# Performance work log

Measured on AMD Instinct MI355X. Metric: run time of the kernel, lower is better.

## Reference

```python
import jax, jax.numpy as jnp
import numpy as np

D_IN = 1024
D_OUT = 1024
SEQ = 4096


def setup_inputs() -> dict:
    key = jax.random.key(0)
    kx, kq, kk, kv = jax.random.split(key, 4)
    s = 1.0 / np.sqrt(D_IN)
    return {
        "x": jax.random.normal(kx, (SEQ, D_IN), dtype=jnp.float32),
        # torch Linear weights: shape [d_out, d_in], y = x @ W.T
        "Wq": jax.random.uniform(kq, (D_OUT, D_IN), jnp.float32, -s, s),
        "Wk": jax.random.uniform(kk, (D_OUT, D_IN), jnp.float32, -s, s),
        "Wv": jax.random.uniform(kv, (D_OUT, D_IN), jnp.float32, -s, s),
    }


def reference(x, Wq, Wk, Wv):
    # QKV projections (no bias)
    q = x @ Wq.T  # [N, d_out]
    k = x @ Wk.T
    v = x @ Wv.T
    scale = 1.0 / jnp.sqrt(jnp.asarray(k.shape[-1], x.dtype))
    att = jax.nn.softmax((q @ k.T) * scale, axis=-1)  # [N, N]
    return att @ v  # [N, d_out]
```

## Files before the change

### kernel.cpp

```cpp
#include <hip/hip_runtime.h>
#include <hip/hip_bf16.h>
#include <math.h>

typedef __attribute__((ext_vector_type(8))) short short8;
typedef __attribute__((ext_vector_type(4))) float floatx4;

static __device__ __forceinline__ unsigned short f2bf(float f) {
    union { float f; unsigned int u; } a; a.f = f;
    unsigned int u = a.u;
    return (unsigned short)((u + 0x7FFFu + ((u >> 16) & 1u)) >> 16);
}

static __device__ __forceinline__ void cvt8(const float* __restrict__ src,
                                            unsigned short* __restrict__ dst, int i) {
    float4 v0 = *(const float4*)(src + i);
    float4 v1 = *(const float4*)(src + i + 4);
    ushort4 o0, o1;
    o0.x = f2bf(v0.x); o0.y = f2bf(v0.y); o0.z = f2bf(v0.z); o0.w = f2bf(v0.w);
    o1.x = f2bf(v1.x); o1.y = f2bf(v1.y); o1.z = f2bf(v1.z); o1.w = f2bf(v1.w);
    *(ushort4*)(dst + i) = o0;
    *(ushort4*)(dst + i + 4) = o1;
}

__global__ __launch_bounds__(256)
void cvt_f32_bf16(const float* __restrict__ src, unsigned short* __restrict__ dst, int n) {
    int i = (blockIdx.x * 256 + threadIdx.x) * 8;
    if (i < n) cvt8(src, dst, i);
}

struct W3 { const float* s[3]; unsigned short* d[3]; };
__global__ __launch_bounds__(256)
void cvt_w3(W3 a, int n) {
    int i = (blockIdx.x * 256 + threadIdx.x) * 8;
    if (i < n) cvt8(a.s[blockIdx.z], a.d[blockIdx.z], i);
}

__global__ __launch_bounds__(256)
void zero_f32(float* __restrict__ p) { p[blockIdx.x * 256 + threadIdx.x] = 0.f; }

template<int BM, int BN, int TI, int TJ, int WCOLS>
__device__ __forceinline__ void gemm_core(const unsigned short* __restrict__ A,
                                          const unsigned short* __restrict__ B,
                                          int lda, int k_begin, int k_end,
                                          unsigned short* sA, unsigned short* sB,
                                          floatx4 (&acc)[TI][TJ],
                                          int bm, int bn)
{
    const int t    = threadIdx.x;
    const int wave = t >> 6;
    const int lane = t & 63;
    const int wm = (wave / WCOLS) * (TI * 16);
    const int wn = (wave % WCOLS) * (TJ * 16);

    const int srow   = t >> 3;
    const int schunk = t & 7;
    const int gchunk = schunk ^ (srow & 7);
    const int lm  = lane & 15;
    const int swz = lm & 7;

    for (int k0 = k_begin; k0 < k_end; k0 += 64) {
        __syncthreads();
        #pragma unroll
        for (int r = 0; r < BM / 32; r++) {
            const unsigned short* gA =
                A + (size_t)(bm + srow + r * 32) * lda + k0 + gchunk * 8;
            __builtin_amdgcn_global_load_lds(
                (const __attribute__((address_space(1))) void*)gA,
                (__attribute__((address_space(3))) void*)((char*)sA + wave * 1024 + r * 4096),
                16, 0, 0);
        }
        #pragma unroll
        for (int r = 0; r < BN / 32; r++) {
            const unsigned short* gB =
                B + (size_t)(bn + srow + r * 32) * lda + k0 + gchunk * 8;
            __builtin_amdgcn_global_load_lds(
                (const __attribute__((address_space(1))) void*)gB,
                (__attribute__((address_space(3))) void*)((char*)sB + wave * 1024 + r * 4096),
                16, 0, 0);
        }
        __syncthreads();

        #pragma unroll
        for (int kk = 0; kk < 64; kk += 32) {
            const int c  = (kk >> 3) + (lane >> 4);
            const int ce = ((c ^ swz) << 3);
            short8 a_frag[TI], b_frag[TJ];
            #pragma unroll
            for (int i = 0; i < TI; i++)
                a_frag[i] = *(const short8*)&sA[(wm + i * 16 + lm) * 64 + ce];
            #pragma unroll
            for (int j = 0; j < TJ; j++)
                b_frag[j] = *(const short8*)&sB[(wn + j * 16 + lm) * 64 + ce];
            #pragma unroll
            for (int i = 0; i < TI; i++)
                #pragma unroll
                for (int j = 0; j < TJ; j++)
                    acc[i][j] = __builtin_amdgcn_mfma_f32_16x16x32_bf16(
                        a_frag[i], b_frag[j], acc[i][j], 0, 0, 0);
        }
    }
}


struct P3 { const unsigned short* W[3]; unsigned short* O[3]; };
__global__ __launch_bounds__(256)
void proj3(const unsigned short* __restrict__ xb, P3 a) {
    __shared__ unsigned short sA[64 * 64];
    __shared__ unsigned short sB[128 * 64];
    const int z = blockIdx.z;
    const unsigned short* B = a.W[z];
    unsigned short* O = a.O[z];
    const bool trans = (z == 2);
    const int ldc = trans ? 4096 : 1024;

    floatx4 acc[4][2];
    #pragma unroll
    for (int i = 0; i < 4; i++)
        #pragma unroll
        for (int j = 0; j < 2; j++) { floatx4 zz = {0.f,0.f,0.f,0.f}; acc[i][j] = zz; }

    const int bm = blockIdx.y * 64, bn = blockIdx.x * 128;
    gemm_core<64, 128, 4, 2, 4>(xb, B, 1024, 0, 1024, sA, sB, acc, bm, bn);

    const int lane = threadIdx.x & 63, wave = threadIdx.x >> 6;
    const int wn = (wave & 3) * 32;
    const int lm = lane & 15, rq = (lane >> 4) * 4;
    #pragma unroll
    for (int i = 0; i < 4; i++)
        #pragma unroll
        for (int j = 0; j < 2; j++) {
            int tm = bm + i * 16 + rq;
            int tn = bn + wn + j * 16 + lm;
            #pragma unroll
            for (int r = 0; r < 4; r++) {
                unsigned short h = f2bf(acc[i][j][r]);
                size_t idx = trans ? ((size_t)tn * ldc + (tm + r))
                                   : ((size_t)(tm + r) * ldc + tn);
                O[idx] = h;
            }
        }
}

__global__ __launch_bounds__(256)
void gemm_ps(const unsigned short* __restrict__ q, const unsigned short* __restrict__ k,
             unsigned short* __restrict__ Pm, float* __restrict__ l) {
    __shared__ unsigned short sA[128 * 64];
    __shared__ unsigned short sB[128 * 64];

    floatx4 acc[4][4];
    #pragma unroll
    for (int i = 0; i < 4; i++)
        #pragma unroll
        for (int j = 0; j < 4; j++) { floatx4 zz = {0.f,0.f,0.f,0.f}; acc[i][j] = zz; }

    const int bm = blockIdx.y * 128, bn = blockIdx.x * 128;
    gemm_core<128, 128, 4, 4, 2>(q, k, 1024, 0, 1024, sA, sB, acc, bm, bn);

    const int lane = threadIdx.x & 63, wave = threadIdx.x >> 6;
    const int wm = (wave >> 1) * 64, wn = (wave & 1) * 64;
    const int lm = lane & 15, rq = (lane >> 4) * 4;
    #pragma unroll
    for (int i = 0; i < 4; i++) {
        #pragma unroll
        for (int r = 0; r < 4; r++) {
            int row = bm + wm + i * 16 + rq + r;
            float rs = 0.f;
            #pragma unroll
            for (int j = 0; j < 4; j++) {
                float e = __expf(acc[i][j][r] * 0.03125f);
                rs += e;
                int tn = bn + wn + j * 16 + lm;
                Pm[(size_t)row * 4096 + tn] = f2bf(e);
            }
            rs += __shfl_xor(rs, 1);
            rs += __shfl_xor(rs, 2);
            rs += __shfl_xor(rs, 4);
            rs += __shfl_xor(rs, 8);
            if (lm == 0) atomicAdd(l + row, rs);
        }
    }
}

__global__ __launch_bounds__(256)
void gemm_osplit(const unsigned short* __restrict__ Pm, const unsigned short* __restrict__ vT,
                 float* __restrict__ Opart) {
    __shared__ unsigned short sA[64 * 64];
    __shared__ unsigned short sB[128 * 64];

    floatx4 acc[4][2];
    #pragma unroll
    for (int i = 0; i < 4; i++)
        #pragma unroll
        for (int j = 0; j < 2; j++) { floatx4 zz = {0.f,0.f,0.f,0.f}; acc[i][j] = zz; }

    const int z = blockIdx.z;
    const int bm = blockIdx.y * 64, bn = blockIdx.x * 128;
    gemm_core<64, 128, 4, 2, 4>(Pm, vT, 4096, z * 2048, (z + 1) * 2048, sA, sB, acc, bm, bn);

    float* Op = Opart + (size_t)z * (4096 * 1024);
    const int lane = threadIdx.x & 63, wave = threadIdx.x >> 6;
    const int wn = (wave & 3) * 32;
    const int lm = lane & 15, rq = (lane >> 4) * 4;
    #pragma unroll
    for (int i = 0; i < 4; i++)
        #pragma unroll
        for (int j = 0; j < 2; j++) {
            int tm = bm + i * 16 + rq;
            int tn = bn + wn + j * 16 + lm;
            #pragma unroll
            for (int r = 0; r < 4; r++)
                Op[(size_t)(tm + r) * 1024 + tn] = acc[i][j][r];
        }
}

__global__ __launch_bounds__(256)
void reduce_scale(const float* __restrict__ Op, const float* __restrict__ l,
                  float* __restrict__ out) {
    int i = (blockIdx.x * 256 + threadIdx.x) * 4;
    float4 a = *(const float4*)(Op + i);
    float4 b = *(const float4*)(Op + 4096 * 1024 + i);
    float inv = 1.0f / l[i >> 10];
    float4 o;
    o.x = (a.x + b.x) * inv; o.y = (a.y + b.y) * inv;
    o.z = (a.z + b.z) * inv; o.w = (a.w + b.w) * inv;
    *(float4*)(out + i) = o;
}

extern "C" void kernel_launch(void* const* d_in, const int* in_sizes, int n_in,
                              void* d_out, int out_size, void* d_ws, size_t ws_size,
                              hipStream_t stream) {
    const float* x  = (const float*)d_in[0];
    const float* Wq = (const float*)d_in[1];
    const float* Wk = (const float*)d_in[2];
    const float* Wv = (const float*)d_in[3];
    float* out = (float*)d_out;

    const int SEQ = 4096, D = 1024;
    char* ws = (char*)d_ws;
    const size_t MB = 1u << 20;
    unsigned short* vTb = (unsigned short*)(ws);
    unsigned short* xb  = (unsigned short*)(ws + 8 * MB);
    unsigned short* Wqb = (unsigned short*)(ws + 16 * MB);
    unsigned short* Wkb = (unsigned short*)(ws + 18 * MB);
    unsigned short* Wvb = (unsigned short*)(ws + 20 * MB);
    unsigned short* qb  = (unsigned short*)(ws + 22 * MB);
    unsigned short* kb  = (unsigned short*)(ws + 30 * MB);
    unsigned short* P   = (unsigned short*)(ws + 38 * MB);
    float*          l   = (float*)(ws + 70 * MB);
    float*          Opart = (float*)(ws + 72 * MB);

    dim3 blk(256);
    cvt_f32_bf16<<<(SEQ * D) / 2048, blk, 0, stream>>>(x, xb, SEQ * D);
    W3 w3 = {{Wq, Wk, Wv}, {Wqb, Wkb, Wvb}};
    cvt_w3<<<dim3((D * D) / 2048, 1, 3), blk, 0, stream>>>(w3, D * D);
    zero_f32<<<SEQ / 256, blk, 0, stream>>>(l);

    P3 p3 = {{Wqb, Wkb, Wvb}, {qb, kb, vTb}};
    proj3<<<dim3(D / 128, SEQ / 64, 3), blk, 0, stream>>>(xb, p3);

    gemm_ps<<<dim3(SEQ / 128, SEQ / 128), blk, 0, stream>>>(qb, kb, P, l);

    gemm_osplit<<<dim3(D / 128, SEQ / 64, 2), blk, 0, stream>>>(P, vTb, Opart);

    reduce_scale<<<(SEQ * D) / 1024, blk, 0, stream>>>(Opart, l, out);
}
```

Measured before the change: 236.1 us.

## Use BK=128 k-tiles for attention GEMMs, fold scale into Q, merge zeroing

Adds a K-tile-depth template parameter to the shared GEMM core and raises it to 128 for the QK^T and PV GEMMs, so each main-loop step loads twice as much data and runs half as many barrier pairs. The 1/sqrt(d) softmax scale moves out of the exp epilogue and into the Q projection store. The zeroing of the row-sum buffer is folded into the x conversion kernel as one extra block, which removes a kernel launch. The deeper tiles double LDS use per block, which can lower occupancy, and the swizzle now uses 16 chunks per row.

```diff
diff --git a/kernel.cpp b/kernel.cpp
--- a/kernel.cpp
+++ b/kernel.cpp
@@ -23,7 +23,15 @@
 }
 
 __global__ __launch_bounds__(256)
-void cvt_f32_bf16(const float* __restrict__ src, unsigned short* __restrict__ dst, int n) {
+void cvt_x_zero(const float* __restrict__ src, unsigned short* __restrict__ dst,
+                int n, float* __restrict__ l) {
+    if ((int)blockIdx.x == gridDim.x - 1) {
+        float4 z = {0.f, 0.f, 0.f, 0.f};
+        #pragma unroll
+        for (int c = 0; c < 4; c++)
+            *(float4*)(l + threadIdx.x * 16 + c * 4) = z;
+        return;
+    }
     int i = (blockIdx.x * 256 + threadIdx.x) * 8;
     if (i < n) cvt8(src, dst, i);
 }
@@ -35,10 +43,7 @@
     if (i < n) cvt8(a.s[blockIdx.z], a.d[blockIdx.z], i);
 }
 
-__global__ __launch_bounds__(256)
-void zero_f32(float* __restrict__ p) { p[blockIdx.x * 256 + threadIdx.x] = 0.f; }
-
-template<int BM, int BN, int TI, int TJ, int WCOLS>
+template<int BM, int BN, int BK, int TI, int TJ, int WCOLS>
 __device__ __forceinline__ void gemm_core(const unsigned short* __restrict__ A,
                                           const unsigned short* __restrict__ B,
                                           int lda, int k_begin, int k_end,
@@ -46,33 +51,35 @@
                                           floatx4 (&acc)[TI][TJ],
                                           int bm, int bn)
 {
+    constexpr int CPR = BK / 8;
+    constexpr int RPR = 2048 / BK;
     const int t    = threadIdx.x;
     const int wave = t >> 6;
     const int lane = t & 63;
     const int wm = (wave / WCOLS) * (TI * 16);
     const int wn = (wave % WCOLS) * (TJ * 16);
 
-    const int srow   = t >> 3;
-    const int schunk = t & 7;
-    const int gchunk = schunk ^ (srow & 7);
+    const int srow   = t / CPR;
+    const int schunk = t % CPR;
+    const int gchunk = schunk ^ (srow & (CPR - 1));
     const int lm  = lane & 15;
-    const int swz = lm & 7;
-
-    for (int k0 = k_begin; k0 < k_end; k0 += 64) {
+    const int swz = lm & (CPR - 1);
+
+    for (int k0 = k_begin; k0 < k_end; k0 += BK) {
         __syncthreads();
         #pragma unroll
-        for (int r = 0; r < BM / 32; r++) {
+        for (int r = 0; r < (BM * BK) / 2048; r++) {
             const unsigned short* gA =
-                A + (size_t)(bm + srow + r * 32) * lda + k0 + gchunk * 8;
+                A + (size_t)(bm + srow + r * RPR) * lda + k0 + gchunk * 8;
             __builtin_amdgcn_global_load_lds(
                 (const __attribute__((address_space(1))) void*)gA,
                 (__attribute__((address_space(3))) void*)((char*)sA + wave * 1024 + r * 4096),
                 16, 0, 0);
         }
         #pragma unroll
-        for (int r = 0; r < BN / 32; r++) {
+        for (int r = 0; r < (BN * BK) / 2048; r++) {
             const unsigned short* gB =
-                B + (size_t)(bn + srow + r * 32) * lda + k0 + gchunk * 8;
+                B + (size_t)(bn + srow + r * RPR) * lda + k0 + gchunk * 8;
             __builtin_amdgcn_global_load_lds(
                 (const __attribute__((address_space(1))) void*)gB,
                 (__attribute__((address_space(3))) void*)((char*)sB + wave * 1024 + r * 4096),
@@ -81,16 +88,16 @@
         __syncthreads();
 
         #pragma unroll
-        for (int kk = 0; kk < 64; kk += 32) {
+        for (int kk = 0; kk < BK; kk += 32) {
             const int c  = (kk >> 3) + (lane >> 4);
             const int ce = ((c ^ swz) << 3);
             short8 a_frag[TI], b_frag[TJ];
             #pragma unroll
             for (int i = 0; i < TI; i++)
-                a_frag[i] = *(const short8*)&sA[(wm + i * 16 + lm) * 64 + ce];
+                a_frag[i] = *(const short8*)&sA[(wm + i * 16 + lm) * BK + ce];
             #pragma unroll
             for (int j = 0; j < TJ; j++)
-                b_frag[j] = *(const short8*)&sB[(wn + j * 16 + lm) * 64 + ce];
+                b_frag[j] = *(const short8*)&sB[(wn + j * 16 + lm) * BK + ce];
             #pragma unroll
             for (int i = 0; i < TI; i++)
                 #pragma unroll
@@ -112,6 +119,7 @@
     unsigned short* O = a.O[z];
     const bool trans = (z == 2);
     const int ldc = trans ? 4096 : 1024;
+    const float scale = (z == 0) ? 0.03125f : 1.0f;
 
     floatx4 acc[4][2];
     #pragma unroll
@@ -120,7 +128,7 @@
         for (int j = 0; j < 2; j++) { floatx4 zz = {0.f,0.f,0.f,0.f}; acc[i][j] = zz; }
 
     const int bm = blockIdx.y * 64, bn = blockIdx.x * 128;
-    gemm_core<64, 128, 4, 2, 4>(xb, B, 1024, 0, 1024, sA, sB, acc, bm, bn);
+    gemm_core<64, 128, 64, 4, 2, 4>(xb, B, 1024, 0, 1024, sA, sB, acc, bm, bn);
 
     const int lane = threadIdx.x & 63, wave = threadIdx.x >> 6;
     const int wn = (wave & 3) * 32;
@@ -133,7 +141,7 @@
             int tn = bn + wn + j * 16 + lm;
             #pragma unroll
             for (int r = 0; r < 4; r++) {
-                unsigned short h = f2bf(acc[i][j][r]);
+                unsigned short h = f2bf(acc[i][j][r] * scale);
                 size_t idx = trans ? ((size_t)tn * ldc + (tm + r))
                                    : ((size_t)(tm + r) * ldc + tn);
                 O[idx] = h;
@@ -144,8 +152,8 @@
 __global__ __launch_bounds__(256)
 void gemm_ps(const unsigned short* __restrict__ q, const unsigned short* __restrict__ k,
              unsigned short* __restrict__ Pm, float* __restrict__ l) {
-    __shared__ unsigned short sA[128 * 64];
-    __shared__ unsigned short sB[128 * 64];
+    __shared__ unsigned short sA[128 * 128];
+    __shared__ unsigned short sB[128 * 128];
 
     floatx4 acc[4][4];
     #pragma unroll
@@ -154,7 +162,7 @@
         for (int j = 0; j < 4; j++) { floatx4 zz = {0.f,0.f,0.f,0.f}; acc[i][j] = zz; }
 
     const int bm = blockIdx.y * 128, bn = blockIdx.x * 128;
-    gemm_core<128, 128, 4, 4, 2>(q, k, 1024, 0, 1024, sA, sB, acc, bm, bn);
+    gemm_core<128, 128, 128, 4, 4, 2>(q, k, 1024, 0, 1024, sA, sB, acc, bm, bn);
 
     const int lane = threadIdx.x & 63, wave = threadIdx.x >> 6;
     const int wm = (wave >> 1) * 64, wn = (wave & 1) * 64;
@@ -167,7 +175,7 @@
             float rs = 0.f;
             #pragma unroll
             for (int j = 0; j < 4; j++) {
-                float e = __expf(acc[i][j][r] * 0.03125f);
+                float e = __expf(acc[i][j][r]);
                 rs += e;
                 int tn = bn + wn + j * 16 + lm;
                 Pm[(size_t)row * 4096 + tn] = f2bf(e);
@@ -184,8 +192,8 @@
 __global__ __launch_bounds__(256)
 void gemm_osplit(const unsigned short* __restrict__ Pm, const unsigned short* __restrict__ vT,
                  float* __restrict__ Opart) {
-    __shared__ unsigned short sA[64 * 64];
-    __shared__ unsigned short sB[128 * 64];
+    __shared__ unsigned short sA[64 * 128];
+    __shared__ unsigned short sB[128 * 128];
 
     floatx4 acc[4][2];
     #pragma unroll
@@ -195,7 +203,8 @@
 
     const int z = blockIdx.z;
     const int bm = blockIdx.y * 64, bn = blockIdx.x * 128;
-    gemm_core<64, 128, 4, 2, 4>(Pm, vT, 4096, z * 2048, (z + 1) * 2048, sA, sB, acc, bm, bn);
+    gemm_core<64, 128, 128, 4, 2, 4>(Pm, vT, 4096, z * 2048, (z + 1) * 2048,
+                                     sA, sB, acc, bm, bn);
 
     float* Op = Opart + (size_t)z * (4096 * 1024);
     const int lane = threadIdx.x & 63, wave = threadIdx.x >> 6;
@@ -250,10 +259,9 @@
     float*          Opart = (float*)(ws + 72 * MB);
 
     dim3 blk(256);
-    cvt_f32_bf16<<<(SEQ * D) / 2048, blk, 0, stream>>>(x, xb, SEQ * D);
+    cvt_x_zero<<<(SEQ * D) / 2048 + 1, blk, 0, stream>>>(x, xb, SEQ * D, l);
     W3 w3 = {{Wq, Wk, Wv}, {Wqb, Wkb, Wvb}};
     cvt_w3<<<dim3((D * D) / 2048, 1, 3), blk, 0, stream>>>(w3, D * D);
-    zero_f32<<<SEQ / 256, blk, 0, stream>>>(l);
 
     P3 p3 = {{Wqb, Wkb, Wvb}, {qb, kb, vTb}};
     proj3<<<dim3(D / 128, SEQ / 64, 3), blk, 0, stream>>>(xb, p3);
```

Measured after the change: 236.3 us. Within noise of the previous version (+0.1%).
